# Kernel optimization log

Measured on AMD Instinct MI355X. Metric: run time of the kernel, lower is better.

## Reference

```python
import jax, jax.numpy as jnp
import numpy as np

N, E, B = 100000, 1600000, 128
ND, ED, H, NC = 91, 20, 128, 3
EPS = 1e-5


def setup_inputs() -> dict:
    key = jax.random.key(0)
    ks = jax.random.split(key, 16)
    s = 0.05
    inp = {
        "node_feats": jax.random.normal(ks[0], (N, ND), jnp.float32),
        "edge_index": jax.random.randint(ks[1], (2, E), 0, N, dtype=jnp.int32),
        "edge_feats": jax.random.normal(ks[2], (E, ED), jnp.float32),
        "batch": jnp.sort(jax.random.randint(ks[3], (N,), 0, B, dtype=jnp.int32)),
        # params
        "embed_w": jax.random.normal(ks[4], (ND, H), jnp.float32) * s,
        "embed_b": jnp.zeros((H,), jnp.float32),
        "conv_wsrc": jax.random.normal(ks[5], (NC, H, 2 * H), jnp.float32) * s,
        "conv_wdst": jax.random.normal(ks[6], (NC, H, 2 * H), jnp.float32) * s,
        "conv_we": jax.random.normal(ks[7], (NC, ED, 2 * H), jnp.float32) * s,
        "conv_b": jnp.zeros((NC, 2 * H), jnp.float32),
        "bn_gamma": jnp.ones((NC, H), jnp.float32),
        "bn_beta": jnp.zeros((NC, H), jnp.float32),
        "fc1_w": jax.random.normal(ks[8], (H, H), jnp.float32) * s,
        "fc1_b": jnp.zeros((H,), jnp.float32),
        "fc_bn_gamma": jnp.ones((H,), jnp.float32),
        "fc_bn_beta": jnp.zeros((H,), jnp.float32),
        "out_w": jax.random.normal(ks[9], (H, 1), jnp.float32) * s,
        "out_b": jnp.zeros((1,), jnp.float32),
    }
    return inp


def _bn(x, gamma, beta):
    # training-mode batchnorm over axis 0, biased variance (torch semantics)
    m = x.mean(0)
    v = x.var(0)
    return (x - m) * jax.lax.rsqrt(v + EPS) * gamma + beta


def reference(node_feats, edge_index, edge_feats, batch, embed_w, embed_b,
              conv_wsrc, conv_wdst, conv_we, conv_b, bn_gamma, bn_beta,
              fc1_w, fc1_b, fc_bn_gamma, fc_bn_beta, out_w, out_b):
    h = node_feats @ embed_w + embed_b  # (N, H)
    src, dst = edge_index[0], edge_index[1]
    for i in range(NC):
        # CGCNN gated conv: Linear on concat[h_src, h_dst, e] split into 3 matmuls
        z = (h[src] @ conv_wsrc[i] + h[dst] @ conv_wdst[i]
             + edge_feats @ conv_we[i] + conv_b[i])  # (E, 2H)
        msg = jax.nn.sigmoid(z[:, :H]) * jax.nn.softplus(z[:, H:])
        agg = jax.ops.segment_sum(msg, dst, num_segments=N)  # (N, H)
        h = jax.nn.relu(h + _bn(agg, bn_gamma[i], bn_beta[i]))
    # global mean pool over graphs
    counts = jnp.maximum(
        jax.ops.segment_sum(jnp.ones((h.shape[0], 1), h.dtype), batch, num_segments=B), 1.0)
    g = jax.ops.segment_sum(h, batch, num_segments=B) / counts  # (B, H)
    x = jax.nn.relu(_bn(g @ fc1_w + fc1_b, fc_bn_gamma, fc_bn_beta))
    return x @ out_w + out_b  # (B, 1)
```

## Files before the change

kernel.cpp:

```cpp
#include <hip/hip_runtime.h>
#include <hip/hip_bf16.h>

#define NN 100000
#define EE 1600000
#define HH 128
#define NDIM 91
#define EDIM 20
#define BB 128
#define EPSF 1e-5f
#define NBLK 4096
#define PER 400
#define ECAP (NBLK * PER)
#define LN2I 1.44269504f

typedef __attribute__((ext_vector_type(8))) short short8v;
typedef __attribute__((ext_vector_type(4))) float f32x4;

__device__ __forceinline__ short f2bs(float x) {
  __hip_bfloat16 b = __float2bfloat16(x);
  return *reinterpret_cast<short*>(&b);
}
__device__ __forceinline__ float bl(unsigned int u) {
  union { unsigned int i; float f; } x; x.i = u << 16; return x.f;
}
__device__ __forceinline__ float bh(unsigned int u) {
  union { unsigned int i; float f; } x; x.i = u & 0xffff0000u; return x.f;
}

__global__ __launch_bounds__(256) void k_embed(const float* __restrict__ nf,
                                               const float* __restrict__ W,
                                               const float* __restrict__ b,
                                               float* __restrict__ h) {
  __shared__ float w_s[NDIM * HH];
  __shared__ float b_s[HH];
  __shared__ float a_s[16 * 92];
  for (int i = threadIdx.x; i < NDIM * HH; i += 256) w_s[i] = W[i];
  if (threadIdx.x < HH) b_s[threadIdx.x] = b[threadIdx.x];
  __syncthreads();
  int col = threadIdx.x & 127, rs = threadIdx.x >> 7;
  for (int base = blockIdx.x * 16; base < NN; base += gridDim.x * 16) {
    int nrows = min(16, NN - base);
    int tot = nrows * NDIM;
    for (int i = threadIdx.x; i < tot; i += 256) {
      int r = i / NDIM;
      a_s[r * 92 + (i - r * NDIM)] = nf[(size_t)base * NDIM + i];
    }
    __syncthreads();
    float acc[8];
#pragma unroll
    for (int r = 0; r < 8; r++) acc[r] = 0.f;
    for (int k = 0; k < NDIM; k++) {
      float w = w_s[k * HH + col];
#pragma unroll
      for (int r = 0; r < 8; r++) acc[r] += a_s[(rs * 8 + r) * 92 + k] * w;
    }
#pragma unroll
    for (int r = 0; r < 8; r++) {
      int row = base + rs * 8 + r;
      if (row < NN) h[(size_t)row * HH + col] = acc[r] + b_s[col];
    }
    __syncthreads();
  }
}

__global__ __launch_bounds__(256) void k_w2bf(const float* __restrict__ Wsrc,
                                              const float* __restrict__ Wdst,
                                              short* __restrict__ wt) {
  int i = blockIdx.x * 256 + threadIdx.x;
  if (i >= 2 * 256 * 128) return;
  int mat = i >> 15;
  int r = (i >> 7) & 255;
  int k = i & 127;
  const float* W = mat ? Wdst : Wsrc;
  wt[i] = f2bs(W[k * 256 + r]);
}

__global__ __launch_bounds__(256) void k_we2bf(const float* __restrict__ We,
                                               const float* __restrict__ bias,
                                               short* __restrict__ Web) {
  int i = blockIdx.x * 256 + threadIdx.x;
  if (i >= 256 * 32) return;
  int c = i >> 5, k = i & 31;
  float v = (k < EDIM) ? We[k * 256 + c] : (k == EDIM ? bias[c] : 0.f);
  float sc = (c < 128) ? -LN2I : LN2I;
  Web[i] = f2bs(v * sc);
}

__global__ __launch_bounds__(256) void k_node_mm(float* __restrict__ h,
                                                 const float* __restrict__ agg,
                                                 const float* __restrict__ stats,
                                                 const short* __restrict__ wt,
                                                 unsigned int* __restrict__ hs2,
                                                 unsigned int* __restrict__ hd2,
                                                 int apply) {
  __shared__ short hlds[64 * 128];
  __shared__ float st_s[256];
  int base = blockIdx.x * 64;
  int t = threadIdx.x;
  if (apply) {
    if (t < 256) st_s[t] = stats[t];
    __syncthreads();
  }
#pragma unroll
  for (int p = 0; p < 4; p++) {
    int e0 = (p * 256 + t) * 8;
    int row = e0 >> 7, col = e0 & 127;
    int gr = base + row;
    float4 f0 = make_float4(0.f, 0.f, 0.f, 0.f), f1 = f0;
    if (gr < NN) {
      f0 = *(const float4*)&h[(size_t)gr * 128 + col];
      f1 = *(const float4*)&h[(size_t)gr * 128 + col + 4];
      if (apply) {
        float4 a0 = *(const float4*)&agg[(size_t)gr * 128 + col];
        float4 a1 = *(const float4*)&agg[(size_t)gr * 128 + col + 4];
        f0.x = fmaxf(f0.x + a0.x * st_s[col] + st_s[128 + col], 0.f);
        f0.y = fmaxf(f0.y + a0.y * st_s[col + 1] + st_s[129 + col], 0.f);
        f0.z = fmaxf(f0.z + a0.z * st_s[col + 2] + st_s[130 + col], 0.f);
        f0.w = fmaxf(f0.w + a0.w * st_s[col + 3] + st_s[131 + col], 0.f);
        f1.x = fmaxf(f1.x + a1.x * st_s[col + 4] + st_s[132 + col], 0.f);
        f1.y = fmaxf(f1.y + a1.y * st_s[col + 5] + st_s[133 + col], 0.f);
        f1.z = fmaxf(f1.z + a1.z * st_s[col + 6] + st_s[134 + col], 0.f);
        f1.w = fmaxf(f1.w + a1.w * st_s[col + 7] + st_s[135 + col], 0.f);
        *(float4*)&h[(size_t)gr * 128 + col] = f0;
        *(float4*)&h[(size_t)gr * 128 + col + 4] = f1;
      }
    }
    short8v u;
    u[0] = f2bs(f0.x); u[1] = f2bs(f0.y); u[2] = f2bs(f0.z); u[3] = f2bs(f0.w);
    u[4] = f2bs(f1.x); u[5] = f2bs(f1.y); u[6] = f2bs(f1.z); u[7] = f2bs(f1.w);
    *(short8v*)&hlds[e0] = u;
  }
  __syncthreads();
  int w = t >> 6, l = t & 63;
  int cl = l & 15, kg = l >> 4;
  short8v a[4];
#pragma unroll
  for (int kk = 0; kk < 4; kk++)
    a[kk] = *(const short8v*)&hlds[(w * 16 + cl) * 128 + kk * 32 + kg * 8];
#pragma unroll
  for (int mat = 0; mat < 2; mat++) {
    const short* wtm = wt + mat * 256 * 128;
    unsigned int* out = mat ? hd2 : hs2;
    f32x4 acc[16];
#pragma unroll
    for (int ct = 0; ct < 16; ct++) acc[ct] = (f32x4)(0.f);
#pragma unroll
    for (int ct = 0; ct < 16; ct++) {
#pragma unroll
      for (int kk = 0; kk < 4; kk++) {
        short8v b = *(const short8v*)&wtm[(ct * 16 + cl) * 128 + kk * 32 + kg * 8];
        acc[ct] = __builtin_amdgcn_mfma_f32_16x16x32_bf16(a[kk], b, acc[ct], 0, 0, 0);
      }
    }
#pragma unroll
    for (int ct = 0; ct < 8; ct++) {
#pragma unroll
      for (int r = 0; r < 4; r++) {
        int gr = base + w * 16 + kg * 4 + r;
        if (gr < NN) {
          unsigned short g = (unsigned short)f2bs(-LN2I * acc[ct][r]);
          unsigned short s = (unsigned short)f2bs(LN2I * acc[ct + 8][r]);
          int slot = (ct >> 1) * 32 + (cl << 1) + (ct & 1);
          out[(size_t)gr * 128 + slot] = (unsigned int)g | ((unsigned int)s << 16);
        }
      }
    }
  }
}

__global__ __launch_bounds__(256) void k_hist(const int* __restrict__ dst,
                                              int* __restrict__ cnt) {
  for (int e = blockIdx.x * 256 + threadIdx.x; e < EE; e += gridDim.x * 256)
    atomicAdd(&cnt[dst[e]], 1);
}

__global__ __launch_bounds__(1024) void k_scan(const int* __restrict__ cnt,
                                               int* __restrict__ off) {
  __shared__ int ps[1024];
  int t = threadIdx.x;
  const int R = (NN + 1023) / 1024;
  int b0 = t * R, b1 = min(NN, b0 + R);
  int s = 0;
  for (int i = b0; i < b1; i++) s += cnt[i];
  ps[t] = s;
  __syncthreads();
  for (int d = 1; d < 1024; d <<= 1) {
    int v = (t >= d) ? ps[t - d] : 0;
    __syncthreads();
    ps[t] += v;
    __syncthreads();
  }
  int run = (t == 0) ? 0 : ps[t - 1];
  for (int i = b0; i < b1; i++) {
    off[i] = run;
    run += cnt[i];
  }
}

__global__ __launch_bounds__(256) void k_scatter(const int* __restrict__ src,
                                                 const int* __restrict__ dst,
                                                 const float* __restrict__ ef,
                                                 int* __restrict__ off,
                                                 int* __restrict__ src_s,
                                                 int* __restrict__ dst_s,
                                                 short* __restrict__ efp) {
  for (int e = blockIdx.x * 256 + threadIdx.x; e < EE; e += gridDim.x * 256) {
    int d = dst[e];
    int pos = atomicAdd(&off[d], 1);
    src_s[pos] = src[e];
    dst_s[pos] = d;
    const float4* in = (const float4*)&ef[(size_t)e * EDIM];
    float4 q0 = in[0], q1 = in[1], q2 = in[2], q3 = in[3], q4 = in[4];
    short8v u0, u1, u2, u3;
    u0[0] = f2bs(q0.x); u0[1] = f2bs(q0.y); u0[2] = f2bs(q0.z); u0[3] = f2bs(q0.w);
    u0[4] = f2bs(q1.x); u0[5] = f2bs(q1.y); u0[6] = f2bs(q1.z); u0[7] = f2bs(q1.w);
    u1[0] = f2bs(q2.x); u1[1] = f2bs(q2.y); u1[2] = f2bs(q2.z); u1[3] = f2bs(q2.w);
    u1[4] = f2bs(q3.x); u1[5] = f2bs(q3.y); u1[6] = f2bs(q3.z); u1[7] = f2bs(q3.w);
    u2[0] = f2bs(q4.x); u2[1] = f2bs(q4.y); u2[2] = f2bs(q4.z); u2[3] = f2bs(q4.w);
    u2[4] = f2bs(1.0f); u2[5] = 0; u2[6] = 0; u2[7] = 0;
    u3 = (short8v)(short)0;
    short8v* op = (short8v*)&efp[(size_t)pos * 32];
    op[0] = u0; op[1] = u1; op[2] = u2; op[3] = u3;
  }
}

__global__ __launch_bounds__(256) void k_padtail(int* __restrict__ src_s,
                                                 int* __restrict__ dst_s,
                                                 short* __restrict__ efp) {
  int e = EE + blockIdx.x * 256 + threadIdx.x;
  if (e >= ECAP) return;
  src_s[e] = 0;
  dst_s[e] = -2;
  short8v z = (short8v)(short)0;
  short8v* op = (short8v*)&efp[(size_t)e * 32];
  op[0] = z; op[1] = z; op[2] = z; op[3] = z;
}

__global__ __launch_bounds__(256) void k_edge_v6(
    const unsigned int* __restrict__ hs2, const unsigned int* __restrict__ hd2,
    const short* __restrict__ efp, const int* __restrict__ srcp,
    const int* __restrict__ dstp, const short* __restrict__ Web,
    float* __restrict__ agg) {
  const int i0 = blockIdx.x * PER;
  int t = threadIdx.x;
  int w = t >> 6, l = t & 63, cl = l & 15, kg = l >> 4;
  int c0 = w * 32 + cl, c1 = c0 + 16;
  int pairoff = w * 32 + (cl << 1);
  short8v bg0 = *(const short8v*)&Web[c0 * 32 + kg * 8];
  short8v bg1 = *(const short8v*)&Web[c1 * 32 + kg * 8];
  short8v bs0 = *(const short8v*)&Web[(128 + c0) * 32 + kg * 8];
  short8v bs1 = *(const short8v*)&Web[(128 + c1) * 32 + kg * 8];
  int cur = -1;
  float acc0 = 0.f, acc1 = 0.f;
  float hg0 = 0.f, hp0 = 0.f, hg1 = 0.f, hp1 = 0.f;
  const int o_a_base = i0 + (cl >> 2) * 100 + (cl & 3);
  const int o_e_base = i0 + kg * 100;
  for (int it = 0; it < 25; ++it) {
    int off4 = it * 4;
    short8v a = *(const short8v*)&efp[(size_t)(o_a_base + off4) * 32 + kg * 8];
    f32x4 zgv0 = __builtin_amdgcn_mfma_f32_16x16x32_bf16(a, bg0, (f32x4)(0.f), 0, 0, 0);
    f32x4 zgv1 = __builtin_amdgcn_mfma_f32_16x16x32_bf16(a, bg1, (f32x4)(0.f), 0, 0, 0);
    f32x4 zsv0 = __builtin_amdgcn_mfma_f32_16x16x32_bf16(a, bs0, (f32x4)(0.f), 0, 0, 0);
    f32x4 zsv1 = __builtin_amdgcn_mfma_f32_16x16x32_bf16(a, bs1, (f32x4)(0.f), 0, 0, 0);
    int o_e = o_e_base + off4;
    int4 s4 = *(const int4*)&srcp[o_e];
    int4 d4 = *(const int4*)&dstp[o_e];
    int ss[4] = {s4.x, s4.y, s4.z, s4.w};
    int dd[4] = {d4.x, d4.y, d4.z, d4.w};
#pragma unroll
    for (int r = 0; r < 4; ++r) {
      int s = ss[r], d = dd[r];
      if (d != cur) {
        if (cur >= 0) {
          atomicAdd(&agg[cur * HH + c0], acc0);
          atomicAdd(&agg[cur * HH + c1], acc1);
        }
        acc0 = 0.f; acc1 = 0.f;
        cur = d;
        if (d >= 0) {
          uint2 x = *(const uint2*)&hd2[((size_t)d << 7) + pairoff];
          hg0 = bl(x.x); hp0 = bh(x.x);
          hg1 = bl(x.y); hp1 = bh(x.y);
        }
      }
      uint2 u = *(const uint2*)&hs2[((size_t)s << 7) + pairoff];
      float zgN0 = zgv0[r] + bl(u.x) + hg0;
      float zsp0 = zsv0[r] + bh(u.x) + hp0;
      float zgN1 = zgv1[r] + bl(u.y) + hg1;
      float zsp1 = zsv1[r] + bh(u.y) + hp1;
      float sp0 = __builtin_amdgcn_logf(1.f + __builtin_amdgcn_exp2f(zsp0));
      float sp1 = __builtin_amdgcn_logf(1.f + __builtin_amdgcn_exp2f(zsp1));
      acc0 += sp0 * __builtin_amdgcn_rcpf(1.f + __builtin_amdgcn_exp2f(zgN0));
      acc1 += sp1 * __builtin_amdgcn_rcpf(1.f + __builtin_amdgcn_exp2f(zgN1));
    }
  }
  if (cur >= 0) {
    atomicAdd(&agg[cur * HH + c0], acc0);
    atomicAdd(&agg[cur * HH + c1], acc1);
  }
}

__global__ __launch_bounds__(256) void k_bn_stats(const float* __restrict__ agg,
                                                  float* __restrict__ stats) {
  int col = threadIdx.x & 127, hlf = threadIdx.x >> 7;
  float s = 0.f, sq = 0.f;
  for (int row = blockIdx.x * 2 + hlf; row < NN; row += gridDim.x * 2) {
    float v = agg[(size_t)row * HH + col];
    s += v; sq += v * v;
  }
  __shared__ float ls[256], lq[256];
  ls[threadIdx.x] = s; lq[threadIdx.x] = sq;
  __syncthreads();
  if (hlf == 0) {
    atomicAdd(&stats[col], ls[col] + ls[col + 128]);
    atomicAdd(&stats[128 + col], lq[col] + lq[col + 128]);
  }
}

__global__ void k_bn_fin(float* stats, const float* __restrict__ gam,
                         const float* __restrict__ bet) {
  int c = threadIdx.x;
  if (c >= HH) return;
  float mean = stats[c] / (float)NN;
  float var = stats[HH + c] / (float)NN - mean * mean;
  float sc = rsqrtf(var + EPSF) * gam[c];
  stats[c] = sc;
  stats[HH + c] = bet[c] - mean * sc;
}

__global__ __launch_bounds__(256) void k_update(float* __restrict__ h,
                                                const float* __restrict__ agg,
                                                const float* __restrict__ stats) {
  for (size_t i = (size_t)blockIdx.x * blockDim.x + threadIdx.x; i < (size_t)NN * HH;
       i += (size_t)gridDim.x * blockDim.x) {
    int c = (int)(i & 127);
    float v = h[i] + agg[i] * stats[c] + stats[128 + c];
    h[i] = fmaxf(v, 0.f);
  }
}

__global__ void k_pool(const float* __restrict__ h, const int* __restrict__ batch,
                       float* __restrict__ g, float* __restrict__ gcnt) {
  int col = threadIdx.x;
  int chunk = (NN + gridDim.x - 1) / gridDim.x;
  int n0 = blockIdx.x * chunk, n1 = min(NN, n0 + chunk);
  if (n0 >= n1) return;
  int cur = batch[n0];
  float acc = 0.f, cnt = 0.f;
  for (int n = n0; n < n1; n++) {
    int bb = batch[n];
    if (bb != cur) {
      atomicAdd(&g[cur * HH + col], acc);
      if (col == 0) atomicAdd(&gcnt[cur], cnt);
      acc = 0.f; cnt = 0.f; cur = bb;
    }
    acc += h[(size_t)n * HH + col];
    cnt += 1.f;
  }
  atomicAdd(&g[cur * HH + col], acc);
  if (col == 0) atomicAdd(&gcnt[cur], cnt);
}

__global__ __launch_bounds__(256) void k_final(float* __restrict__ g,
                                               const float* __restrict__ gcnt,
                                               const float* __restrict__ fc1w,
                                               const float* __restrict__ fc1b,
                                               const float* __restrict__ gam,
                                               const float* __restrict__ bet,
                                               const float* __restrict__ ow,
                                               const float* __restrict__ ob,
                                               float* __restrict__ out) {
  __shared__ float w_s[HH * HH];
  __shared__ float y_s[BB * HH];
  __shared__ float ls[256], lq[256];
  for (int i = threadIdx.x; i < HH * HH; i += 256) w_s[i] = fc1w[i];
  for (int i = threadIdx.x; i < BB * HH; i += 256) {
    int r = i >> 7;
    g[i] = g[i] / fmaxf(gcnt[r], 1.f);
  }
  __syncthreads();
  int c = threadIdx.x & 127, h2 = threadIdx.x >> 7;
  for (int rr = 0; rr < 64; rr++) {
    int r = h2 * 64 + rr;
    float acc = fc1b[c];
    for (int k = 0; k < HH; k++) acc += g[r * HH + k] * w_s[k * HH + c];
    y_s[r * HH + c] = acc;
  }
  __syncthreads();
  float s = 0.f, sq = 0.f;
  for (int rr = 0; rr < 64; rr++) {
    float v = y_s[(h2 * 64 + rr) * HH + c];
    s += v; sq += v * v;
  }
  ls[threadIdx.x] = s; lq[threadIdx.x] = sq;
  __syncthreads();
  if (h2 == 0) {
    float ss = ls[c] + ls[c + 128], qq = lq[c] + lq[c + 128];
    float mean = ss / (float)BB, var = qq / (float)BB - mean * mean;
    float sc = rsqrtf(var + EPSF) * gam[c];
    ls[c] = sc;
    lq[c] = bet[c] - mean * sc;
  }
  __syncthreads();
  for (int rr = 0; rr < 64; rr++) {
    int r = h2 * 64 + rr;
    y_s[r * HH + c] = fmaxf(y_s[r * HH + c] * ls[c] + lq[c], 0.f);
  }
  __syncthreads();
  int r2 = threadIdx.x >> 1, hf = threadIdx.x & 1;
  float acc = 0.f;
  for (int k = hf * 64; k < hf * 64 + 64; k++) acc += y_s[r2 * HH + k] * ow[k];
  __syncthreads();
  ls[threadIdx.x] = acc;
  __syncthreads();
  if (hf == 0) out[r2] = ls[threadIdx.x] + ls[threadIdx.x + 1] + ob[0];
}

extern "C" void kernel_launch(void* const* d_in, const int* in_sizes, int n_in,
                              void* d_out, int out_size, void* d_ws, size_t ws_size,
                              hipStream_t stream) {
  (void)in_sizes; (void)n_in; (void)out_size; (void)ws_size;
  const float* node_feats = (const float*)d_in[0];
  const int* edge_index = (const int*)d_in[1];
  const float* edge_feats = (const float*)d_in[2];
  const int* batch = (const int*)d_in[3];
  const float* embed_w = (const float*)d_in[4];
  const float* embed_b = (const float*)d_in[5];
  const float* conv_wsrc = (const float*)d_in[6];
  const float* conv_wdst = (const float*)d_in[7];
  const float* conv_we = (const float*)d_in[8];
  const float* conv_b = (const float*)d_in[9];
  const float* bn_gamma = (const float*)d_in[10];
  const float* bn_beta = (const float*)d_in[11];
  const float* fc1_w = (const float*)d_in[12];
  const float* fc1_b = (const float*)d_in[13];
  const float* fc_bn_gamma = (const float*)d_in[14];
  const float* fc_bn_beta = (const float*)d_in[15];
  const float* out_w = (const float*)d_in[16];
  const float* out_b = (const float*)d_in[17];

  char* ws = (char*)d_ws;
  size_t o = 0;
  float* h = (float*)(ws + o);              o += (size_t)NN * HH * 4;
  unsigned int* hs2 = (unsigned int*)(ws + o); o += (size_t)NN * 128 * 4;
  unsigned int* hd2 = (unsigned int*)(ws + o); o += (size_t)NN * 128 * 4;
  float* agg = (float*)(ws + o);            o += (size_t)NN * HH * 4;
  short* efp = (short*)(ws + o);            o += (size_t)ECAP * 32 * 2;
  int* src_s = (int*)(ws + o);              o += (size_t)ECAP * 4;
  int* dst_s = (int*)(ws + o);              o += (size_t)ECAP * 4;
  int* cnt = (int*)(ws + o);                o += (size_t)NN * 4;
  int* off = (int*)(ws + o);                o += (size_t)NN * 4;
  short* wt = (short*)(ws + o);             o += (size_t)2 * 256 * 128 * 2;
  short* Web = (short*)(ws + o);            o += (size_t)256 * 32 * 2;
  float* stats = (float*)(ws + o);          o += 256 * 4;
  float* g = (float*)(ws + o);              o += (size_t)BB * HH * 4;
  float* gcnt = (float*)(ws + o);           o += BB * 4;

  const int* src = edge_index;
  const int* dst = edge_index + EE;

  hipMemsetAsync(cnt, 0, (size_t)NN * 4, stream);
  k_hist<<<2048, 256, 0, stream>>>(dst, cnt);
  k_scan<<<1, 1024, 0, stream>>>(cnt, off);
  k_scatter<<<2048, 256, 0, stream>>>(src, dst, edge_feats, off, src_s, dst_s, efp);
  k_padtail<<<(ECAP - EE + 255) / 256, 256, 0, stream>>>(src_s, dst_s, efp);

  k_embed<<<512, 256, 0, stream>>>(node_feats, embed_w, embed_b, h);

  for (int i = 0; i < 3; i++) {
    k_w2bf<<<256, 256, 0, stream>>>(conv_wsrc + (size_t)i * HH * 256,
                                    conv_wdst + (size_t)i * HH * 256, wt);
    k_we2bf<<<32, 256, 0, stream>>>(conv_we + (size_t)i * EDIM * 256,
                                    conv_b + (size_t)i * 256, Web);
    k_node_mm<<<(NN + 63) / 64, 256, 0, stream>>>(h, agg, stats, wt, hs2, hd2,
                                                  i > 0 ? 1 : 0);
    hipMemsetAsync(agg, 0, (size_t)NN * HH * 4, stream);
    hipMemsetAsync(stats, 0, 256 * 4, stream);
    k_edge_v6<<<NBLK, 256, 0, stream>>>(hs2, hd2, efp, src_s, dst_s, Web, agg);
    k_bn_stats<<<1024, 256, 0, stream>>>(agg, stats);
    k_bn_fin<<<1, 128, 0, stream>>>(stats, bn_gamma + i * HH, bn_beta + i * HH);
  }
  k_update<<<2048, 256, 0, stream>>>(h, agg, stats);

  hipMemsetAsync(g, 0, (size_t)BB * HH * 4, stream);
  hipMemsetAsync(gcnt, 0, BB * 4, stream);
  k_pool<<<256, 128, 0, stream>>>(h, batch, g, gcnt);
  k_final<<<1, 256, 0, stream>>>(g, gcnt, fc1_w, fc1_b, fc_bn_gamma, fc_bn_beta,
                                 out_w, out_b, (float*)d_out);
}
```

Before: 2.033 ms.

## Fuse weight prep, drop BN atomics and final update, remap edge blocks

```diff
diff --git a/kernel.cpp b/kernel.cpp
--- a/kernel.cpp
+++ b/kernel.cpp
@@ -12,6 +12,7 @@
 #define PER 400
 #define ECAP (NBLK * PER)
 #define LN2I 1.44269504f
+#define NPART 512
 
 typedef __attribute__((ext_vector_type(8))) short short8v;
 typedef __attribute__((ext_vector_type(4))) float f32x4;
@@ -63,27 +64,26 @@
   }
 }
 
-__global__ __launch_bounds__(256) void k_w2bf(const float* __restrict__ Wsrc,
-                                              const float* __restrict__ Wdst,
-                                              short* __restrict__ wt) {
-  int i = blockIdx.x * 256 + threadIdx.x;
-  if (i >= 2 * 256 * 128) return;
-  int mat = i >> 15;
-  int r = (i >> 7) & 255;
-  int k = i & 127;
-  const float* W = mat ? Wdst : Wsrc;
-  wt[i] = f2bs(W[k * 256 + r]);
-}
-
-__global__ __launch_bounds__(256) void k_we2bf(const float* __restrict__ We,
+__global__ __launch_bounds__(256) void k_wprep(const float* __restrict__ Wsrc,
+                                               const float* __restrict__ Wdst,
+                                               const float* __restrict__ We,
                                                const float* __restrict__ bias,
+                                               short* __restrict__ wt,
                                                short* __restrict__ Web) {
   int i = blockIdx.x * 256 + threadIdx.x;
-  if (i >= 256 * 32) return;
-  int c = i >> 5, k = i & 31;
-  float v = (k < EDIM) ? We[k * 256 + c] : (k == EDIM ? bias[c] : 0.f);
-  float sc = (c < 128) ? -LN2I : LN2I;
-  Web[i] = f2bs(v * sc);
+  if (i < 2 * 256 * 128) {
+    int mat = i >> 15;
+    int r = (i >> 7) & 255;
+    int k = i & 127;
+    const float* W = mat ? Wdst : Wsrc;
+    wt[i] = f2bs(W[k * 256 + r]);
+  } else if (i < 2 * 256 * 128 + 256 * 32) {
+    int j = i - 2 * 256 * 128;
+    int c = j >> 5, k = j & 31;
+    float v = (k < EDIM) ? We[k * 256 + c] : (k == EDIM ? bias[c] : 0.f);
+    float sc = (c < 128) ? -LN2I : LN2I;
+    Web[j] = f2bs(v * sc);
+  }
 }
 
 __global__ __launch_bounds__(256) void k_node_mm(float* __restrict__ h,
@@ -153,15 +153,19 @@
       }
     }
 #pragma unroll
-    for (int ct = 0; ct < 8; ct++) {
+    for (int j = 0; j < 4; j++) {
 #pragma unroll
       for (int r = 0; r < 4; r++) {
         int gr = base + w * 16 + kg * 4 + r;
         if (gr < NN) {
-          unsigned short g = (unsigned short)f2bs(-LN2I * acc[ct][r]);
-          unsigned short s = (unsigned short)f2bs(LN2I * acc[ct + 8][r]);
-          int slot = (ct >> 1) * 32 + (cl << 1) + (ct & 1);
-          out[(size_t)gr * 128 + slot] = (unsigned int)g | ((unsigned int)s << 16);
+          unsigned short g0 = (unsigned short)f2bs(-LN2I * acc[2 * j][r]);
+          unsigned short s0 = (unsigned short)f2bs(LN2I * acc[2 * j + 8][r]);
+          unsigned short g1 = (unsigned short)f2bs(-LN2I * acc[2 * j + 1][r]);
+          unsigned short s1 = (unsigned short)f2bs(LN2I * acc[2 * j + 9][r]);
+          uint2 val;
+          val.x = (unsigned int)g0 | ((unsigned int)s0 << 16);
+          val.y = (unsigned int)g1 | ((unsigned int)s1 << 16);
+          *(uint2*)&out[(size_t)gr * 128 + j * 32 + (cl << 1)] = val;
         }
       }
     }
@@ -236,12 +240,13 @@
   op[0] = z; op[1] = z; op[2] = z; op[3] = z;
 }
 
-__global__ __launch_bounds__(256) void k_edge_v6(
+__global__ __launch_bounds__(256) void k_edge_v7(
     const unsigned int* __restrict__ hs2, const unsigned int* __restrict__ hd2,
     const short* __restrict__ efp, const int* __restrict__ srcp,
     const int* __restrict__ dstp, const short* __restrict__ Web,
     float* __restrict__ agg) {
-  const int i0 = blockIdx.x * PER;
+  int bid = ((blockIdx.x & 7) << 9) | (blockIdx.x >> 3);
+  const int i0 = bid * PER;
   int t = threadIdx.x;
   int w = t >> 6, l = t & 63, cl = l & 15, kg = l >> 4;
   int c0 = w * 32 + cl, c1 = c0 + 16;
@@ -301,10 +306,10 @@
 }
 
 __global__ __launch_bounds__(256) void k_bn_stats(const float* __restrict__ agg,
-                                                  float* __restrict__ stats) {
+                                                  float* __restrict__ part) {
   int col = threadIdx.x & 127, hlf = threadIdx.x >> 7;
   float s = 0.f, sq = 0.f;
-  for (int row = blockIdx.x * 2 + hlf; row < NN; row += gridDim.x * 2) {
+  for (int row = blockIdx.x * 2 + hlf; row < NN; row += NPART * 2) {
     float v = agg[(size_t)row * HH + col];
     s += v; sq += v * v;
   }
@@ -312,36 +317,32 @@
   ls[threadIdx.x] = s; lq[threadIdx.x] = sq;
   __syncthreads();
   if (hlf == 0) {
-    atomicAdd(&stats[col], ls[col] + ls[col + 128]);
-    atomicAdd(&stats[128 + col], lq[col] + lq[col + 128]);
-  }
-}
-
-__global__ void k_bn_fin(float* stats, const float* __restrict__ gam,
-                         const float* __restrict__ bet) {
+    part[(size_t)blockIdx.x * 256 + col] = ls[col] + ls[col + 128];
+    part[(size_t)blockIdx.x * 256 + 128 + col] = lq[col] + lq[col + 128];
+  }
+}
+
+__global__ void k_bn_fin(const float* __restrict__ part, float* __restrict__ stats,
+                         const float* __restrict__ gam, const float* __restrict__ bet) {
   int c = threadIdx.x;
   if (c >= HH) return;
-  float mean = stats[c] / (float)NN;
-  float var = stats[HH + c] / (float)NN - mean * mean;
+  float s = 0.f, q = 0.f;
+  for (int b = 0; b < NPART; b++) {
+    s += part[(size_t)b * 256 + c];
+    q += part[(size_t)b * 256 + 128 + c];
+  }
+  float mean = s / (float)NN;
+  float var = q / (float)NN - mean * mean;
   float sc = rsqrtf(var + EPSF) * gam[c];
   stats[c] = sc;
   stats[HH + c] = bet[c] - mean * sc;
 }
 
-__global__ __launch_bounds__(256) void k_update(float* __restrict__ h,
-                                                const float* __restrict__ agg,
-                                                const float* __restrict__ stats) {
-  for (size_t i = (size_t)blockIdx.x * blockDim.x + threadIdx.x; i < (size_t)NN * HH;
-       i += (size_t)gridDim.x * blockDim.x) {
-    int c = (int)(i & 127);
-    float v = h[i] + agg[i] * stats[c] + stats[128 + c];
-    h[i] = fmaxf(v, 0.f);
-  }
-}
-
-__global__ void k_pool(const float* __restrict__ h, const int* __restrict__ batch,
+__global__ void k_pool(const float* __restrict__ h, const float* __restrict__ agg,
+                       const float* __restrict__ stats, const int* __restrict__ batch,
                        float* __restrict__ g, float* __restrict__ gcnt) {
   int col = threadIdx.x;
+  float sc = stats[col], sh = stats[128 + col];
   int chunk = (NN + gridDim.x - 1) / gridDim.x;
   int n0 = blockIdx.x * chunk, n1 = min(NN, n0 + chunk);
   if (n0 >= n1) return;
@@ -354,7 +355,7 @@
       if (col == 0) atomicAdd(&gcnt[cur], cnt);
       acc = 0.f; cnt = 0.f; cur = bb;
     }
-    acc += h[(size_t)n * HH + col];
+    acc += fmaxf(h[(size_t)n * HH + col] + agg[(size_t)n * HH + col] * sc + sh, 0.f);
     cnt += 1.f;
   }
   atomicAdd(&g[cur * HH + col], acc);
@@ -452,6 +453,7 @@
   int* off = (int*)(ws + o);                o += (size_t)NN * 4;
   short* wt = (short*)(ws + o);             o += (size_t)2 * 256 * 128 * 2;
   short* Web = (short*)(ws + o);            o += (size_t)256 * 32 * 2;
+  float* part = (float*)(ws + o);           o += (size_t)NPART * 256 * 4;
   float* stats = (float*)(ws + o);          o += 256 * 4;
   float* g = (float*)(ws + o);              o += (size_t)BB * HH * 4;
   float* gcnt = (float*)(ws + o);           o += BB * 4;
@@ -468,23 +470,21 @@
   k_embed<<<512, 256, 0, stream>>>(node_feats, embed_w, embed_b, h);
 
   for (int i = 0; i < 3; i++) {
-    k_w2bf<<<256, 256, 0, stream>>>(conv_wsrc + (size_t)i * HH * 256,
-                                    conv_wdst + (size_t)i * HH * 256, wt);
-    k_we2bf<<<32, 256, 0, stream>>>(conv_we + (size_t)i * EDIM * 256,
-                                    conv_b + (size_t)i * 256, Web);
+    k_wprep<<<288, 256, 0, stream>>>(conv_wsrc + (size_t)i * HH * 256,
+                                     conv_wdst + (size_t)i * HH * 256,
+                                     conv_we + (size_t)i * EDIM * 256,
+                                     conv_b + (size_t)i * 256, wt, Web);
     k_node_mm<<<(NN + 63) / 64, 256, 0, stream>>>(h, agg, stats, wt, hs2, hd2,
                                                   i > 0 ? 1 : 0);
     hipMemsetAsync(agg, 0, (size_t)NN * HH * 4, stream);
-    hipMemsetAsync(stats, 0, 256 * 4, stream);
-    k_edge_v6<<<NBLK, 256, 0, stream>>>(hs2, hd2, efp, src_s, dst_s, Web, agg);
-    k_bn_stats<<<1024, 256, 0, stream>>>(agg, stats);
-    k_bn_fin<<<1, 128, 0, stream>>>(stats, bn_gamma + i * HH, bn_beta + i * HH);
-  }
-  k_update<<<2048, 256, 0, stream>>>(h, agg, stats);
+    k_edge_v7<<<NBLK, 256, 0, stream>>>(hs2, hd2, efp, src_s, dst_s, Web, agg);
+    k_bn_stats<<<NPART, 256, 0, stream>>>(agg, part);
+    k_bn_fin<<<1, 128, 0, stream>>>(part, stats, bn_gamma + i * HH, bn_beta + i * HH);
+  }
 
   hipMemsetAsync(g, 0, (size_t)BB * HH * 4, stream);
   hipMemsetAsync(gcnt, 0, BB * 4, stream);
-  k_pool<<<256, 128, 0, stream>>>(h, batch, g, gcnt);
+  k_pool<<<256, 128, 0, stream>>>(h, agg, stats, batch, g, gcnt);
   k_final<<<1, 256, 0, stream>>>(g, gcnt, fc1_w, fc1_b, fc_bn_gamma, fc_bn_beta,
                                  out_w, out_b, (float*)d_out);
 }
```

Result: slower. 2.077 ms (+2.2%).
